# Kernel tuning notes

Hardware: AMD Instinct MI355X
Metric: run time of the kernel (lower is better)

The kernel has to match this reference:

```python
import jax, jax.numpy as jnp
import numpy as np

N, E = 20000, 160000
NODE_DIM, EDGE_DIM, H, STEPS = 64, 16, 32, 3


def setup_inputs() -> dict:
    key = jax.random.key(0)
    ks = jax.random.split(key, 10)
    node_feat = jax.random.normal(ks[0], (N, NODE_DIM), dtype=jnp.float32)
    edge_index = jax.random.randint(ks[1], (2, E), 0, N, dtype=jnp.int32)
    edge_feat = jax.random.normal(ks[2], (E, EDGE_DIM), dtype=jnp.float32)
    # node_proj: Linear(node_dim, hidden)
    W_np = jax.random.normal(ks[3], (H, NODE_DIM), dtype=jnp.float32) / np.sqrt(NODE_DIM)
    b_np = jnp.zeros((H,), dtype=jnp.float32)
    # edge_net: Linear(edge_dim, hidden*hidden) -> reshape [E, H, H]
    W_e = jax.random.normal(ks[4], (H * H, EDGE_DIM), dtype=jnp.float32) / np.sqrt(EDGE_DIM)
    b_e = jnp.zeros((H * H,), dtype=jnp.float32)
    # GRUCell params (torch layout: [3H, H], gate order r, z, n)
    W_ih = jax.random.normal(ks[5], (3 * H, H), dtype=jnp.float32) / np.sqrt(H)
    W_hh = jax.random.normal(ks[6], (3 * H, H), dtype=jnp.float32) / np.sqrt(H)
    b_ih = jnp.zeros((3 * H,), dtype=jnp.float32)
    b_hh = jnp.zeros((3 * H,), dtype=jnp.float32)
    return {
        "node_feat": node_feat, "edge_index": edge_index, "edge_feat": edge_feat,
        "W_np": W_np, "b_np": b_np, "W_e": W_e, "b_e": b_e,
        "W_ih": W_ih, "W_hh": W_hh, "b_ih": b_ih, "b_hh": b_hh,
    }


def _gru_cell(x, h, W_ih, W_hh, b_ih, b_hh):
    gi = x @ W_ih.T + b_ih  # [N, 3H]
    gh = h @ W_hh.T + b_hh
    ir, iz, inn = jnp.split(gi, 3, axis=-1)
    hr, hz, hn = jnp.split(gh, 3, axis=-1)
    r = jax.nn.sigmoid(ir + hr)
    z = jax.nn.sigmoid(iz + hz)
    n = jnp.tanh(inn + r * hn)
    return (1.0 - z) * n + z * h


def reference(node_feat, edge_index, edge_feat, W_np, b_np, W_e, b_e, W_ih, W_hh, b_ih, b_hh):
    h = node_feat @ W_np.T + b_np                      # [N, H]
    A = (edge_feat @ W_e.T + b_e).reshape(-1, H, H)    # [E, H, H] per-edge matrices
    src, dst = edge_index[0], edge_index[1]
    for _ in range(STEPS):
        # m[v] += A[e] @ h[src[e]]  -> batched matvec + scatter-add
        msg = jnp.einsum('ehk,ek->eh', A, h[src])      # [E, H]
        m = jax.ops.segment_sum(msg, dst, num_segments=N)
        h = _gru_cell(m, h, W_ih, W_hh, b_ih, b_hh)
    return h
```

## Files before the change

kernel.cpp:

```cpp
#include <hip/hip_runtime.h>
#include <math.h>

#define N_NODES 20000
#define N_EDGES 160000
#define NODE_DIM 64
#define EDGE_DIM 16
#define H 32
#define STEPS 3

__global__ void hist_src_kernel(const int* __restrict__ ei, int* __restrict__ deg) {
    int e = blockIdx.x * 256 + threadIdx.x;
    if (e < N_EDGES) atomicAdd(&deg[ei[e]], 1);
}

__global__ void scan_a_kernel(const int* __restrict__ deg,
                              int* __restrict__ part, int* __restrict__ bsum) {
    __shared__ int s[256];
    int v = blockIdx.x * 256 + threadIdx.x;
    int x = (v < N_NODES) ? deg[v] : 0;
    s[threadIdx.x] = x;
    __syncthreads();
    for (int off = 1; off < 256; off <<= 1) {
        int t = (threadIdx.x >= off) ? s[threadIdx.x - off] : 0;
        __syncthreads();
        s[threadIdx.x] += t;
        __syncthreads();
    }
    if (v < N_NODES) part[v] = s[threadIdx.x] - x;
    if (threadIdx.x == 255) bsum[blockIdx.x] = s[255];
}

__global__ void scan_b_kernel(int* __restrict__ rowptr,
                              const int* __restrict__ bsum,
                              int* __restrict__ cursor) {
    __shared__ int boff[80];
    if (threadIdx.x == 0) {
        int run = 0;
        for (int b = 0; b < 79; ++b) { boff[b] = run; run += bsum[b]; }
    }
    __syncthreads();
    for (int v = threadIdx.x; v < N_NODES; v += 256) {
        int r = rowptr[v] + boff[v >> 8];
        rowptr[v] = r;
        cursor[v] = r;
    }
    if (threadIdx.x == 0) rowptr[N_NODES] = N_EDGES;
}

__global__ void fill_src_kernel(const int* __restrict__ ei, int* __restrict__ cursor,
                                int* __restrict__ eperm, int* __restrict__ src2,
                                int* __restrict__ dst2) {
    int e = blockIdx.x * 256 + threadIdx.x;
    if (e < N_EDGES) {
        int s = ei[e];
        int slot = atomicAdd(&cursor[s], 1);
        eperm[slot] = e;
        src2[slot]  = s;
        dst2[slot]  = ei[N_EDGES + e];
    }
}

__global__ void permute_ef_kernel(const float* __restrict__ ef,
                                  const int* __restrict__ eperm,
                                  float* __restrict__ ef2) {
    int t = blockIdx.x * 256 + threadIdx.x;
    if (t < N_EDGES * EDGE_DIM) {
        int j = t >> 4;
        int d = t & 15;
        ef2[t] = ef[eperm[j] * EDGE_DIM + d];
    }
}

__global__ void node_proj_kernel(const float* __restrict__ nf,
                                 const float* __restrict__ W,
                                 const float* __restrict__ b,
                                 float* __restrict__ h) {
    int tid = blockIdx.x * blockDim.x + threadIdx.x;
    if (tid >= N_NODES * H) return;
    int v = tid >> 5;
    int i = tid & 31;
    const float* __restrict__ row = nf + v * NODE_DIM;
    const float* __restrict__ w   = W + i * NODE_DIM;
    float acc = b[i];
#pragma unroll
    for (int d = 0; d < NODE_DIM; ++d) acc = fmaf(row[d], w[d], acc);
    h[tid] = acc;
}

__global__ __launch_bounds__(576)
void fused_msg_kernel(const float* __restrict__ We,
                      const float* __restrict__ be,
                      const float* __restrict__ h,
                      const int* __restrict__ rowptr,
                      const int* __restrict__ src2,
                      const int* __restrict__ dst2,
                      const float* __restrict__ ef2,
                      float* __restrict__ m) {
    __shared__ float hs[16 * 32];
    __shared__ float Ul[16 * 576];

    int t = threadIdx.x;

    float wreg[32];
    int p = -1;
    if (t < 512) {
        int L = t >> 4, q = (t >> 2) & 3, e = t & 3;
        int d = t & 15;
#pragma unroll
        for (int k = 0; k < H; ++k) wreg[k] = We[(L * H + k) * EDGE_DIM + d];
        p = q * 136 + L * 4 + e;
    } else if (t < 544) {
        int i = t - 512;
#pragma unroll
        for (int k = 0; k < H; ++k) wreg[k] = be[i * H + k];
        p = 544 + i;
    }

    int v0 = blockIdx.x * 16;

    if (t < 512) hs[t] = h[(size_t)v0 * H + t];
    __syncthreads();

    if (p >= 0) {
        for (int n = 0; n < 16; n += 2) {
            const float4* __restrict__ hp0 = (const float4*)(hs + n * H);
            const float4* __restrict__ hp1 = (const float4*)(hs + (n + 1) * H);
            float a0 = 0.f, a1 = 0.f;
#pragma unroll
            for (int kk = 0; kk < 8; ++kk) {
                float4 q0 = hp0[kk];
                float4 q1 = hp1[kk];
                a0 = fmaf(wreg[4 * kk + 0], q0.x, a0);
                a1 = fmaf(wreg[4 * kk + 0], q1.x, a1);
                a0 = fmaf(wreg[4 * kk + 1], q0.y, a0);
                a1 = fmaf(wreg[4 * kk + 1], q1.y, a1);
                a0 = fmaf(wreg[4 * kk + 2], q0.z, a0);
                a1 = fmaf(wreg[4 * kk + 2], q1.z, a1);
                a0 = fmaf(wreg[4 * kk + 3], q0.w, a0);
                a1 = fmaf(wreg[4 * kk + 3], q1.w, a1);
            }
            Ul[n * 576 + p]       = a0;
            Ul[(n + 1) * 576 + p] = a1;
        }
    }
    __syncthreads();

    int hw   = t >> 5;
    int lane = t & 31;
    int jbeg = rowptr[v0];
    int jend = rowptr[v0 + 16];
    for (int j = jbeg + hw; j < jend; j += 18) {
        int s  = src2[j];
        int ls = s - v0;
        int dd = dst2[j];

        float efv = (lane < EDGE_DIM) ? ef2[(size_t)j * EDGE_DIM + lane] : 0.f;

        const float*  __restrict__ Ur = Ul + ls * 576;
        const float4* __restrict__ up = (const float4*)Ur;
        float4 u0 = up[0 * 34 + lane];
        float4 u1 = up[1 * 34 + lane];
        float4 u2 = up[2 * 34 + lane];
        float4 u3 = up[3 * 34 + lane];
        float msg = Ur[544 + lane];

        msg = fmaf(__shfl(efv,  0, 32), u0.x, msg);
        msg = fmaf(__shfl(efv,  1, 32), u0.y, msg);
        msg = fmaf(__shfl(efv,  2, 32), u0.z, msg);
        msg = fmaf(__shfl(efv,  3, 32), u0.w, msg);
        msg = fmaf(__shfl(efv,  4, 32), u1.x, msg);
        msg = fmaf(__shfl(efv,  5, 32), u1.y, msg);
        msg = fmaf(__shfl(efv,  6, 32), u1.z, msg);
        msg = fmaf(__shfl(efv,  7, 32), u1.w, msg);
        msg = fmaf(__shfl(efv,  8, 32), u2.x, msg);
        msg = fmaf(__shfl(efv,  9, 32), u2.y, msg);
        msg = fmaf(__shfl(efv, 10, 32), u2.z, msg);
        msg = fmaf(__shfl(efv, 11, 32), u2.w, msg);
        msg = fmaf(__shfl(efv, 12, 32), u3.x, msg);
        msg = fmaf(__shfl(efv, 13, 32), u3.y, msg);
        msg = fmaf(__shfl(efv, 14, 32), u3.z, msg);
        msg = fmaf(__shfl(efv, 15, 32), u3.w, msg);

        atomicAdd(&m[(size_t)dd * H + lane], msg);
    }
}

__global__ __launch_bounds__(256, 4)
void gru_kernel(const float* __restrict__ Wih,
                const float* __restrict__ Whh,
                const float* __restrict__ bih,
                const float* __restrict__ bhh,
                float* __restrict__ m,
                const float* __restrict__ h,
                float* __restrict__ hout) {
    __shared__ float xs[16 * 64];
    __shared__ float gs[16 * 32 * 5];

    int c = threadIdx.x & 127;
    float4 wc[16];
    if (c < 96) {
        const float4* p = (const float4*)(Wih + c * H);
#pragma unroll
        for (int q = 0; q < 8; ++q) wc[q] = p[q];
    } else {
#pragma unroll
        for (int q = 0; q < 8; ++q) wc[q] = make_float4(0.f, 0.f, 0.f, 0.f);
    }
    int hrow = (c < 64) ? c : ((c >= 96) ? (c - 32) : -1);
    if (hrow >= 0) {
        const float4* p = (const float4*)(Whh + hrow * H);
#pragma unroll
        for (int q = 0; q < 8; ++q) wc[8 + q] = p[q];
    } else {
#pragma unroll
        for (int q = 0; q < 8; ++q) wc[8 + q] = make_float4(0.f, 0.f, 0.f, 0.f);
    }
    float bias;
    if (c < 64)      bias = bih[c] + bhh[c];
    else if (c < 96) bias = bih[c];
    else             bias = bhh[c - 32];

    int g    = threadIdx.x >> 5;
    int lane = threadIdx.x & 31;
    int half = threadIdx.x >> 7;
    int ci   = c & 31;
    int gt   = c >> 5;

    int v0 = blockIdx.x * 16;
    {
#pragma unroll
        for (int nn = 0; nn < 2; ++nn) {
            int n = g + nn * 8;
            int v = v0 + n;
            float mv = m[(size_t)v * H + lane];
            m[(size_t)v * H + lane] = 0.f;
            xs[n * 64 + lane]      = mv;
            xs[n * 64 + 32 + lane] = h[(size_t)v * H + lane];
        }
        __syncthreads();

#pragma unroll
        for (int n = 0; n < 8; n += 2) {
            const float4* x0 = (const float4*)(xs + (half * 8 + n) * 64);
            const float4* x1 = (const float4*)(xs + (half * 8 + n + 1) * 64);
            float acc0 = bias, acc1 = bias;
#pragma unroll
            for (int q = 0; q < 16; ++q) {
                float4 w = wc[q];
                float4 a = x0[q];
                float4 b = x1[q];
                acc0 = fmaf(w.x, a.x, acc0); acc1 = fmaf(w.x, b.x, acc1);
                acc0 = fmaf(w.y, a.y, acc0); acc1 = fmaf(w.y, b.y, acc1);
                acc0 = fmaf(w.z, a.z, acc0); acc1 = fmaf(w.z, b.z, acc1);
                acc0 = fmaf(w.w, a.w, acc0); acc1 = fmaf(w.w, b.w, acc1);
            }
            gs[((half * 8 + n)     * 32 + ci) * 5 + gt] = acc0;
            gs[((half * 8 + n + 1) * 32 + ci) * 5 + gt] = acc1;
        }
        __syncthreads();

        for (int t = threadIdx.x; t < 16 * 32; t += 256) {
            int nl = t >> 5, ii = t & 31;
            const float* gp = gs + (size_t)t * 5;
            float rs = gp[0], zs = gp[1], in_ = gp[2], hn = gp[3];
            float hv = xs[nl * 64 + 32 + ii];
            float r   = 1.f / (1.f + __expf(-rs));
            float z   = 1.f / (1.f + __expf(-zs));
            float nn2 = tanhf(in_ + r * hn);
            hout[(size_t)(v0 + nl) * H + ii] = (1.f - z) * nn2 + z * hv;
        }
    }
}

extern "C" void kernel_launch(void* const* d_in, const int* in_sizes, int n_in,
                              void* d_out, int out_size, void* d_ws, size_t ws_size,
                              hipStream_t stream) {
    const float* node_feat = (const float*)d_in[0];
    const int*   edge_idx  = (const int*)  d_in[1];
    const float* edge_feat = (const float*)d_in[2];
    const float* W_np      = (const float*)d_in[3];
    const float* b_np      = (const float*)d_in[4];
    const float* W_e       = (const float*)d_in[5];
    const float* b_e       = (const float*)d_in[6];
    const float* W_ih      = (const float*)d_in[7];
    const float* W_hh      = (const float*)d_in[8];
    const float* b_ih      = (const float*)d_in[9];
    const float* b_hh      = (const float*)d_in[10];

    float* h      = (float*)d_ws;
    float* m      = h + (size_t)N_NODES * H;
    float* ef2    = m + (size_t)N_NODES * H;
    int* rowptr   = (int*)(ef2 + (size_t)N_EDGES * EDGE_DIM);
    int* cursor   = rowptr + (N_NODES + 1);
    int* bsum     = cursor + N_NODES;
    int* eperm    = bsum + 80;
    int* src2     = eperm + N_EDGES;
    int* dst2     = src2 + N_EDGES;
    float* out    = (float*)d_out;

    hipMemsetAsync(m, 0, (size_t)N_NODES * H * sizeof(float), stream);
    hipMemsetAsync(cursor, 0, N_NODES * sizeof(int), stream);
    hist_src_kernel<<<(N_EDGES + 255) / 256, 256, 0, stream>>>(edge_idx, cursor);
    scan_a_kernel<<<(N_NODES + 255) / 256, 256, 0, stream>>>(cursor, rowptr, bsum);
    scan_b_kernel<<<1, 256, 0, stream>>>(rowptr, bsum, cursor);
    fill_src_kernel<<<(N_EDGES + 255) / 256, 256, 0, stream>>>(edge_idx, cursor,
                                                               eperm, src2, dst2);
    permute_ef_kernel<<<(N_EDGES * EDGE_DIM + 255) / 256, 256, 0, stream>>>(
        edge_feat, eperm, ef2);

    node_proj_kernel<<<(N_NODES * H + 255) / 256, 256, 0, stream>>>(
        node_feat, W_np, b_np, h);

    for (int step = 0; step < STEPS; ++step) {
        fused_msg_kernel<<<N_NODES / 16, 576, 0, stream>>>(
            W_e, b_e, h, rowptr, src2, dst2, ef2, m);
        float* dst_h = (step == STEPS - 1) ? out : h;
        gru_kernel<<<N_NODES / 16, 256, 0, stream>>>(W_ih, W_hh, b_ih, b_hh,
                                                     m, h, dst_h);
    }
}
```

Baseline: 312.4 us.

## Assign one wave per source node in message kernel and drop shared staging

The message kernel now gives each 64-lane wave one source node at a time. Lanes hold 8 of that node's U coefficients in registers and split the 16 edge features across lane pairs, combining the pair with a shuffle-xor, so the per-edge src index array and the per-edge LDS reloads of U go away. The h staging in shared memory is removed from both the message and GRU kernels, which now read h and m straight from global memory, and m is zeroed in the GRU epilogue. The trade-offs are that only 9 of the 16 nodes per block are handled per pass, which risks load imbalance across waves, half the lanes sit idle during the atomics, and the unstaged per-element global reads may coalesce poorly.

```diff
diff --git a/kernel.cpp b/kernel.cpp
--- a/kernel.cpp
+++ b/kernel.cpp
@@ -48,14 +48,12 @@
 }
 
 __global__ void fill_src_kernel(const int* __restrict__ ei, int* __restrict__ cursor,
-                                int* __restrict__ eperm, int* __restrict__ src2,
-                                int* __restrict__ dst2) {
+                                int* __restrict__ eperm, int* __restrict__ dst2) {
     int e = blockIdx.x * 256 + threadIdx.x;
     if (e < N_EDGES) {
         int s = ei[e];
         int slot = atomicAdd(&cursor[s], 1);
         eperm[slot] = e;
-        src2[slot]  = s;
         dst2[slot]  = ei[N_EDGES + e];
     }
 }
@@ -92,23 +90,20 @@
                       const float* __restrict__ be,
                       const float* __restrict__ h,
                       const int* __restrict__ rowptr,
-                      const int* __restrict__ src2,
                       const int* __restrict__ dst2,
                       const float* __restrict__ ef2,
                       float* __restrict__ m) {
-    __shared__ float hs[16 * 32];
     __shared__ float Ul[16 * 576];
-
-    int t = threadIdx.x;
+    int t  = threadIdx.x;
+    int v0 = blockIdx.x * 16;
 
     float wreg[32];
     int p = -1;
     if (t < 512) {
-        int L = t >> 4, q = (t >> 2) & 3, e = t & 3;
-        int d = t & 15;
+        int L = t >> 4, d = t & 15;
 #pragma unroll
         for (int k = 0; k < H; ++k) wreg[k] = We[(L * H + k) * EDGE_DIM + d];
-        p = q * 136 + L * 4 + e;
+        p = t;
     } else if (t < 544) {
         int i = t - 512;
 #pragma unroll
@@ -116,28 +111,15 @@
         p = 544 + i;
     }
 
-    int v0 = blockIdx.x * 16;
-
-    if (t < 512) hs[t] = h[(size_t)v0 * H + t];
-    __syncthreads();
-
     if (p >= 0) {
         for (int n = 0; n < 16; n += 2) {
-            const float4* __restrict__ hp0 = (const float4*)(hs + n * H);
-            const float4* __restrict__ hp1 = (const float4*)(hs + (n + 1) * H);
+            const float* __restrict__ h0 = h + (size_t)(v0 + n) * H;
+            const float* __restrict__ h1 = h0 + H;
             float a0 = 0.f, a1 = 0.f;
 #pragma unroll
-            for (int kk = 0; kk < 8; ++kk) {
-                float4 q0 = hp0[kk];
-                float4 q1 = hp1[kk];
-                a0 = fmaf(wreg[4 * kk + 0], q0.x, a0);
-                a1 = fmaf(wreg[4 * kk + 0], q1.x, a1);
-                a0 = fmaf(wreg[4 * kk + 1], q0.y, a0);
-                a1 = fmaf(wreg[4 * kk + 1], q1.y, a1);
-                a0 = fmaf(wreg[4 * kk + 2], q0.z, a0);
-                a1 = fmaf(wreg[4 * kk + 2], q1.z, a1);
-                a0 = fmaf(wreg[4 * kk + 3], q0.w, a0);
-                a1 = fmaf(wreg[4 * kk + 3], q1.w, a1);
+            for (int k = 0; k < H; ++k) {
+                a0 = fmaf(wreg[k], h0[k], a0);
+                a1 = fmaf(wreg[k], h1[k], a1);
             }
             Ul[n * 576 + p]       = a0;
             Ul[(n + 1) * 576 + p] = a1;
@@ -145,43 +127,39 @@
     }
     __syncthreads();
 
-    int hw   = t >> 5;
-    int lane = t & 31;
-    int jbeg = rowptr[v0];
-    int jend = rowptr[v0 + 16];
-    for (int j = jbeg + hw; j < jend; j += 18) {
-        int s  = src2[j];
-        int ls = s - v0;
-        int dd = dst2[j];
-
-        float efv = (lane < EDGE_DIM) ? ef2[(size_t)j * EDGE_DIM + lane] : 0.f;
-
-        const float*  __restrict__ Ur = Ul + ls * 576;
-        const float4* __restrict__ up = (const float4*)Ur;
-        float4 u0 = up[0 * 34 + lane];
-        float4 u1 = up[1 * 34 + lane];
-        float4 u2 = up[2 * 34 + lane];
-        float4 u3 = up[3 * 34 + lane];
-        float msg = Ur[544 + lane];
-
-        msg = fmaf(__shfl(efv,  0, 32), u0.x, msg);
-        msg = fmaf(__shfl(efv,  1, 32), u0.y, msg);
-        msg = fmaf(__shfl(efv,  2, 32), u0.z, msg);
-        msg = fmaf(__shfl(efv,  3, 32), u0.w, msg);
-        msg = fmaf(__shfl(efv,  4, 32), u1.x, msg);
-        msg = fmaf(__shfl(efv,  5, 32), u1.y, msg);
-        msg = fmaf(__shfl(efv,  6, 32), u1.z, msg);
-        msg = fmaf(__shfl(efv,  7, 32), u1.w, msg);
-        msg = fmaf(__shfl(efv,  8, 32), u2.x, msg);
-        msg = fmaf(__shfl(efv,  9, 32), u2.y, msg);
-        msg = fmaf(__shfl(efv, 10, 32), u2.z, msg);
-        msg = fmaf(__shfl(efv, 11, 32), u2.w, msg);
-        msg = fmaf(__shfl(efv, 12, 32), u3.x, msg);
-        msg = fmaf(__shfl(efv, 13, 32), u3.y, msg);
-        msg = fmaf(__shfl(efv, 14, 32), u3.z, msg);
-        msg = fmaf(__shfl(efv, 15, 32), u3.w, msg);
-
-        atomicAdd(&m[(size_t)dd * H + lane], msg);
+    int l   = t & 63;
+    int wid = __builtin_amdgcn_readfirstlane(t >> 6);
+    int i   = l >> 1;
+    int dh  = l & 1;
+
+    for (int ls = wid; ls < 16; ls += 9) {
+        const float4* __restrict__ us = (const float4*)(Ul + ls * 576 + l * 8);
+        float4 uA = us[0];
+        float4 uB = us[1];
+        float  bv = Ul[ls * 576 + 544 + i];
+
+        int jb = rowptr[v0 + ls];
+        int je = rowptr[v0 + ls + 1];
+        for (int j = jb; j < je; ++j) {
+            const float4* __restrict__ ep =
+                (const float4*)(ef2 + (size_t)j * EDGE_DIM + dh * 8);
+            float4 ea = ep[0];
+            float4 eb = ep[1];
+            float pp = 0.f;
+            pp = fmaf(ea.x, uA.x, pp);
+            pp = fmaf(ea.y, uA.y, pp);
+            pp = fmaf(ea.z, uA.z, pp);
+            pp = fmaf(ea.w, uA.w, pp);
+            pp = fmaf(eb.x, uB.x, pp);
+            pp = fmaf(eb.y, uB.y, pp);
+            pp = fmaf(eb.z, uB.z, pp);
+            pp = fmaf(eb.w, uB.w, pp);
+            float qq = pp + __shfl_xor(pp, 1, 64);
+            if (dh == 0) {
+                int dd = dst2[j];
+                atomicAdd(&m[(size_t)dd * H + i], bv + qq);
+            }
+        }
     }
 }
 
@@ -193,7 +171,6 @@
                 float* __restrict__ m,
                 const float* __restrict__ h,
                 float* __restrict__ hout) {
-    __shared__ float xs[16 * 64];
     __shared__ float gs[16 * 32 * 5];
 
     int c = threadIdx.x & 127;
@@ -220,55 +197,52 @@
     else if (c < 96) bias = bih[c];
     else             bias = bhh[c - 32];
 
-    int g    = threadIdx.x >> 5;
-    int lane = threadIdx.x & 31;
-    int half = threadIdx.x >> 7;
+    int half = __builtin_amdgcn_readfirstlane(threadIdx.x >> 7);
     int ci   = c & 31;
     int gt   = c >> 5;
-
-    int v0 = blockIdx.x * 16;
-    {
-#pragma unroll
-        for (int nn = 0; nn < 2; ++nn) {
-            int n = g + nn * 8;
-            int v = v0 + n;
-            float mv = m[(size_t)v * H + lane];
-            m[(size_t)v * H + lane] = 0.f;
-            xs[n * 64 + lane]      = mv;
-            xs[n * 64 + 32 + lane] = h[(size_t)v * H + lane];
-        }
-        __syncthreads();
-
-#pragma unroll
-        for (int n = 0; n < 8; n += 2) {
-            const float4* x0 = (const float4*)(xs + (half * 8 + n) * 64);
-            const float4* x1 = (const float4*)(xs + (half * 8 + n + 1) * 64);
-            float acc0 = bias, acc1 = bias;
-#pragma unroll
-            for (int q = 0; q < 16; ++q) {
-                float4 w = wc[q];
-                float4 a = x0[q];
-                float4 b = x1[q];
-                acc0 = fmaf(w.x, a.x, acc0); acc1 = fmaf(w.x, b.x, acc1);
-                acc0 = fmaf(w.y, a.y, acc0); acc1 = fmaf(w.y, b.y, acc1);
-                acc0 = fmaf(w.z, a.z, acc0); acc1 = fmaf(w.z, b.z, acc1);
-                acc0 = fmaf(w.w, a.w, acc0); acc1 = fmaf(w.w, b.w, acc1);
-            }
-            gs[((half * 8 + n)     * 32 + ci) * 5 + gt] = acc0;
-            gs[((half * 8 + n + 1) * 32 + ci) * 5 + gt] = acc1;
-        }
-        __syncthreads();
-
-        for (int t = threadIdx.x; t < 16 * 32; t += 256) {
-            int nl = t >> 5, ii = t & 31;
-            const float* gp = gs + (size_t)t * 5;
-            float rs = gp[0], zs = gp[1], in_ = gp[2], hn = gp[3];
-            float hv = xs[nl * 64 + 32 + ii];
-            float r   = 1.f / (1.f + __expf(-rs));
-            float z   = 1.f / (1.f + __expf(-zs));
-            float nn2 = tanhf(in_ + r * hn);
-            hout[(size_t)(v0 + nl) * H + ii] = (1.f - z) * nn2 + z * hv;
-        }
+    int v0   = blockIdx.x * 16;
+
+#pragma unroll
+    for (int n = 0; n < 8; n += 2) {
+        int v = v0 + half * 8 + n;
+        const float* __restrict__ m0 = m + (size_t)v * H;
+        const float* __restrict__ m1 = m0 + H;
+        const float* __restrict__ h0 = h + (size_t)v * H;
+        const float* __restrict__ h1 = h0 + H;
+        float acc0 = bias, acc1 = bias;
+#pragma unroll
+        for (int q = 0; q < 8; ++q) {
+            float4 w = wc[q];
+            acc0 = fmaf(w.x, m0[q * 4 + 0], acc0); acc1 = fmaf(w.x, m1[q * 4 + 0], acc1);
+            acc0 = fmaf(w.y, m0[q * 4 + 1], acc0); acc1 = fmaf(w.y, m1[q * 4 + 1], acc1);
+            acc0 = fmaf(w.z, m0[q * 4 + 2], acc0); acc1 = fmaf(w.z, m1[q * 4 + 2], acc1);
+            acc0 = fmaf(w.w, m0[q * 4 + 3], acc0); acc1 = fmaf(w.w, m1[q * 4 + 3], acc1);
+        }
+#pragma unroll
+        for (int q = 0; q < 8; ++q) {
+            float4 w = wc[8 + q];
+            acc0 = fmaf(w.x, h0[q * 4 + 0], acc0); acc1 = fmaf(w.x, h1[q * 4 + 0], acc1);
+            acc0 = fmaf(w.y, h0[q * 4 + 1], acc0); acc1 = fmaf(w.y, h1[q * 4 + 1], acc1);
+            acc0 = fmaf(w.z, h0[q * 4 + 2], acc0); acc1 = fmaf(w.z, h1[q * 4 + 2], acc1);
+            acc0 = fmaf(w.w, h0[q * 4 + 3], acc0); acc1 = fmaf(w.w, h1[q * 4 + 3], acc1);
+        }
+        int n0 = half * 8 + n;
+        gs[(n0 * 32 + ci) * 5 + gt]       = acc0;
+        gs[((n0 + 1) * 32 + ci) * 5 + gt] = acc1;
+    }
+    __syncthreads();
+
+    for (int t2 = threadIdx.x; t2 < 16 * 32; t2 += 256) {
+        int nl = t2 >> 5, ii = t2 & 31;
+        int v  = v0 + nl;
+        const float* gp = gs + (size_t)t2 * 5;
+        float rs = gp[0], zs = gp[1], in_ = gp[2], hn = gp[3];
+        float hv = h[(size_t)v * H + ii];
+        float r   = 1.f / (1.f + __expf(-rs));
+        float z   = 1.f / (1.f + __expf(-zs));
+        float nn2 = tanhf(in_ + r * hn);
+        hout[(size_t)v * H + ii] = (1.f - z) * nn2 + z * hv;
+        m[(size_t)v * H + ii]    = 0.f;
     }
 }
 
@@ -294,8 +268,7 @@
     int* cursor   = rowptr + (N_NODES + 1);
     int* bsum     = cursor + N_NODES;
     int* eperm    = bsum + 80;
-    int* src2     = eperm + N_EDGES;
-    int* dst2     = src2 + N_EDGES;
+    int* dst2     = eperm + N_EDGES;
     float* out    = (float*)d_out;
 
     hipMemsetAsync(m, 0, (size_t)N_NODES * H * sizeof(float), stream);
@@ -304,7 +277,7 @@
     scan_a_kernel<<<(N_NODES + 255) / 256, 256, 0, stream>>>(cursor, rowptr, bsum);
     scan_b_kernel<<<1, 256, 0, stream>>>(rowptr, bsum, cursor);
     fill_src_kernel<<<(N_EDGES + 255) / 256, 256, 0, stream>>>(edge_idx, cursor,
-                                                               eperm, src2, dst2);
+                                                               eperm, dst2);
     permute_ef_kernel<<<(N_EDGES * EDGE_DIM + 255) / 256, 256, 0, stream>>>(
         edge_feat, eperm, ef2);
 
@@ -313,7 +286,7 @@
 
     for (int step = 0; step < STEPS; ++step) {
         fused_msg_kernel<<<N_NODES / 16, 576, 0, stream>>>(
-            W_e, b_e, h, rowptr, src2, dst2, ef2, m);
+            W_e, b_e, h, rowptr, dst2, ef2, m);
         float* dst_h = (step == STEPS - 1) ? out : h;
         gru_kernel<<<N_NODES / 16, 256, 0, stream>>>(W_ih, W_hh, b_ih, b_hh,
                                                      m, h, dst_h);
```

After: 330.7 us. 1.06x slower.
